# Kernel optimization log

Hardware: AMD Instinct MI355X
Metric: run time of the kernel (lower is better)

The kernel has to match this reference:

```python
import jax, jax.numpy as jnp
import numpy as np

H, HKV, D, HID = 32, 8, 128, 4096
L, CTX, S = 64, 64, 8192
T = CTX + L
HALF = D // 2
EPS = 1e-6
WP = 4096


def setup_inputs() -> dict:
    key = jax.random.key(0)
    ks = jax.random.split(key, 16)
    f = jnp.float32
    w = 0.02
    return {
        "x": jax.random.normal(ks[0], (1, L, HID), f),
        "x_ctx": jax.random.normal(ks[1], (1, CTX, HID), f),
        "cos_q": jax.random.uniform(ks[2], (1, 1, L, HALF), f, -1.0, 1.0),
        "sin_q": jax.random.uniform(ks[3], (1, 1, L, HALF), f, -1.0, 1.0),
        "cos_k": jax.random.uniform(ks[4], (1, 1, T, HALF), f, -1.0, 1.0),
        "sin_k": jax.random.uniform(ks[5], (1, 1, T, HALF), f, -1.0, 1.0),
        "cache_K_in": jax.random.normal(ks[6], (1, HKV, S, D), f),
        "cache_V_in": jax.random.normal(ks[7], (1, HKV, S, D), f),
        "causal_mask": jnp.ones((1, 1, L, WP + T), dtype=bool),
        "Wq": jax.random.normal(ks[8], (HID, H * D), f) * w,
        "Wk": jax.random.normal(ks[9], (HID, HKV * D), f) * w,
        "Wv": jax.random.normal(ks[10], (HID, HKV * D), f) * w,
        "Wo": jax.random.normal(ks[11], (H * D, HID), f) * w,
        "q_norm_w": jnp.ones((D,), f),
        "k_norm_w": jnp.ones((D,), f),
        "write_pos": WP,
        "rotate": 0,
    }


def _rmsnorm(x, w):
    # normalize over head_dim (last axis)
    var = jnp.mean(x * x, axis=-1, keepdims=True)
    return x * jax.lax.rsqrt(var + EPS) * w


def _rope(x, cos, sin):
    # x: (B, H, T, D); cos/sin: (1, 1, T, HALF) -- rotate-half convention
    x1, x2 = x[..., :HALF], x[..., HALF:]
    return jnp.concatenate([x1 * cos - x2 * sin, x2 * cos + x1 * sin], axis=-1)


def reference(x, x_ctx, cos_q, sin_q, cos_k, sin_k, cache_K_in, cache_V_in,
              causal_mask, Wq, Wk, Wv, Wo, q_norm_w, k_norm_w, write_pos, rotate):
    c = jnp.concatenate([x_ctx, x], axis=1)                  # (1, T, HID)
    q = (x @ Wq).reshape(1, L, H, D)
    k = (c @ Wk).reshape(1, T, HKV, D)
    v = (c @ Wv).reshape(1, T, HKV, D)
    q = _rmsnorm(q, q_norm_w).transpose(0, 2, 1, 3)          # (1, H, L, D)
    k = _rmsnorm(k, k_norm_w).transpose(0, 2, 1, 3)          # (1, HKV, T, D)
    v = v.transpose(0, 2, 1, 3)                               # (1, HKV, T, D)
    q = _rope(q, cos_q, sin_q)
    k = _rope(k, cos_k, sin_k)

    if rotate:  # static Python branch (rotate is a compile-time constant)
        attend_K = jnp.concatenate([cache_K_in[:, :, T:S], k], axis=2)
        attend_V = jnp.concatenate([cache_V_in[:, :, T:S], v], axis=2)
    elif write_pos == 0:
        attend_K, attend_V = k, v
    else:
        attend_K = jnp.concatenate([cache_K_in[:, :, :write_pos], k], axis=2)
        attend_V = jnp.concatenate([cache_V_in[:, :, :write_pos], v], axis=2)

    rep = H // HKV
    scale = jnp.float32(D) ** -0.5
    qg = q.reshape(1, HKV, rep, L, D)
    # grouped attention: broadcast KV heads inline instead of materializing expand
    scores = jnp.einsum('bgrld,bgad->bgrla', qg, attend_K) * scale
    scores = jnp.where(causal_mask[:, :, None], scores, -jnp.inf)  # (1,1,1,L,A) bcast
    probs = jax.nn.softmax(scores, axis=-1)
    o = jnp.einsum('bgrla,bgad->bgrld', probs, attend_V)     # (1, HKV, rep, L, D)
    o = o.reshape(1, H, L, D).transpose(0, 2, 1, 3).reshape(1, L, H * D)
    return (o @ Wo, k, v)
```

## Files before the change

kernel.cpp:

```cpp
#include <hip/hip_runtime.h>

typedef unsigned short u16;
typedef __bf16 bf16x8 __attribute__((ext_vector_type(8)));
typedef float f32x4 __attribute__((ext_vector_type(4)));
typedef u16 u16x8 __attribute__((ext_vector_type(8)));

#define NSPLIT 22
#define KSPLIT 4
#define KC 1024
#define NKT 16
#define OSPLIT 8
#define SCALE_Q 0.08838834764831843f

__device__ __forceinline__ u16 f2bf(float f) {
    unsigned u = __builtin_bit_cast(unsigned, f);
    u += 0x7fff + ((u >> 16) & 1);
    return (u16)(u >> 16);
}
__device__ __forceinline__ float bf2f(u16 h) {
    unsigned u = ((unsigned)h) << 16;
    return __builtin_bit_cast(float, u);
}
__device__ __forceinline__ f32x4 mfma16(bf16x8 a, bf16x8 b, f32x4 c) {
    return __builtin_amdgcn_mfma_f32_16x16x32_bf16(a, b, c, 0, 0, 0);
}

__global__ __launch_bounds__(256)
void k_qkv(const float* __restrict__ x, const float* __restrict__ xctx,
           const float* __restrict__ Wq, const float* __restrict__ Wk,
           const float* __restrict__ Wv, float* __restrict__ part)
{
    const int col0 = blockIdx.x * 32;
    const int ksp = blockIdx.y;
    const int ks0 = ksp * KC;
    const float* W; int ldw, cbase, mat;
    if (col0 < 4096)      { W = Wq; ldw = 4096; cbase = col0;        mat = 0; }
    else if (col0 < 5120) { W = Wk; ldw = 1024; cbase = col0 - 4096; mat = 1; }
    else                  { W = Wv; ldw = 1024; cbase = col0 - 5120; mat = 2; }
    const bool full = (mat != 0);
    const int rowbase = full ? 0 : 64;

    __shared__ __align__(16) u16 As[128][72];
    __shared__ __align__(16) u16 Bs[32 * 64];

    const int t = threadIdx.x;
    const int w = t >> 6, l = t & 63;
    const int lm = l & 15, lg = l >> 4;

    const int arow_base = t >> 4;
    const int akk = (t & 15) << 2;
    const int bk = (t >> 3) << 1;
    const int bn4 = (t & 7) << 2;

    f32x4 pa[8]; f32x4 pb[2];
    f32x4 acc[2][2] = {};

    const float* xr = x - (size_t)64 * 4096;

    #define QKV_LOAD(kt_)                                                      \
    {                                                                          \
        const int kg = ks0 + (kt_) * 64;                                       \
        _Pragma("unroll")                                                      \
        for (int it = 0; it < 4; it++) {                                       \
            int grow = rowbase + it * 16 + arow_base;                          \
            const float* src = (grow < 64) ? (xctx + (size_t)grow * 4096)      \
                                           : (xr + (size_t)grow * 4096);       \
            pa[it] = *(const f32x4*)&src[kg + akk];                            \
        }                                                                      \
        if (full) {                                                            \
            _Pragma("unroll")                                                  \
            for (int it = 4; it < 8; it++) {                                   \
                int grow = it * 16 + arow_base;                                \
                const float* src = (grow < 64) ? (xctx + (size_t)grow * 4096)  \
                                               : (xr + (size_t)grow * 4096);   \
                pa[it] = *(const f32x4*)&src[kg + akk];                        \
            }                                                                  \
        }                                                                      \
        _Pragma("unroll")                                                      \
        for (int e = 0; e < 2; e++)                                            \
            pb[e] = *(const f32x4*)&W[(size_t)(kg + bk + e) * ldw + cbase + bn4]; \
    }

    #define QKV_STORE()                                                        \
    {                                                                          \
        _Pragma("unroll")                                                      \
        for (int it = 0; it < 4; it++) {                                       \
            ushort4 sv; sv.x = f2bf(pa[it][0]); sv.y = f2bf(pa[it][1]);        \
            sv.z = f2bf(pa[it][2]); sv.w = f2bf(pa[it][3]);                    \
            *(ushort4*)&As[it * 16 + arow_base][akk] = sv;                     \
        }                                                                      \
        if (full) {                                                            \
            _Pragma("unroll")                                                  \
            for (int it = 4; it < 8; it++) {                                   \
                ushort4 sv; sv.x = f2bf(pa[it][0]); sv.y = f2bf(pa[it][1]);    \
                sv.z = f2bf(pa[it][2]); sv.w = f2bf(pa[it][3]);                \
                *(ushort4*)&As[it * 16 + arow_base][akk] = sv;                 \
            }                                                                  \
        }                                                                      \
        _Pragma("unroll")                                                      \
        for (int j = 0; j < 4; j++) {                                          \
            int n = bn4 + j;                                                   \
            int idx = n * 64 + (bk ^ (((n >> 1) & 7) << 3));                   \
            ushort2 v2; v2.x = f2bf(pb[0][j]); v2.y = f2bf(pb[1][j]);          \
            *(ushort2*)&Bs[idx] = v2;                                          \
        }                                                                      \
    }

    QKV_LOAD(0);
    #pragma unroll 1
    for (int kt = 0; kt < NKT; kt++) {
        if (kt) __syncthreads();
        QKV_STORE();
        __syncthreads();
        if (kt + 1 < NKT) QKV_LOAD(kt + 1);
        #pragma unroll
        for (int ks = 0; ks < 2; ks++) {
            const int koff = ks * 32 + lg * 8;
            bf16x8 bfr[2];
            #pragma unroll
            for (int nt = 0; nt < 2; nt++) {
                int n = nt * 16 + lm;
                bfr[nt] = *(const bf16x8*)&Bs[n * 64 + (koff ^ (((n >> 1) & 7) << 3))];
            }
            bf16x8 a0 = *(const bf16x8*)&As[w * (full ? 32 : 16) + lm][koff];
            acc[0][0] = mfma16(a0, bfr[0], acc[0][0]);
            acc[0][1] = mfma16(a0, bfr[1], acc[0][1]);
            if (full) {
                bf16x8 a1 = *(const bf16x8*)&As[w * 32 + 16 + lm][koff];
                acc[1][0] = mfma16(a1, bfr[0], acc[1][0]);
                acc[1][1] = mfma16(a1, bfr[1], acc[1][1]);
            }
        }
    }

    const int wrows = full ? 32 : 16;
    const int mts = full ? 2 : 1;
    #pragma unroll
    for (int mt = 0; mt < 2; mt++) {
        if (mt >= mts) break;
        #pragma unroll
        for (int nt = 0; nt < 2; nt++)
            #pragma unroll
            for (int r = 0; r < 4; r++) {
                int grow = rowbase + w * wrows + mt * 16 + lg * 4 + r;
                part[((size_t)ksp * 128 + grow) * 6144 + col0 + nt * 16 + lm] =
                    acc[mt][nt][r];
            }
    }
    #undef QKV_LOAD
    #undef QKV_STORE
}

__global__ __launch_bounds__(256)
void k_normrope(const float* __restrict__ part,
                const float* __restrict__ cosq, const float* __restrict__ sinq,
                const float* __restrict__ cosk, const float* __restrict__ sink,
                const float* __restrict__ qnw, const float* __restrict__ knw,
                u16* __restrict__ qb, u16* __restrict__ kb,
                float* __restrict__ outk, float* __restrict__ outv,
                u16* __restrict__ vbw)
{
    int wid = blockIdx.x * 4 + (threadIdx.x >> 6);
    int lane = threadIdx.x & 63;
    if (wid < 2048) {
        int h = wid >> 6, lq = wid & 63;
        size_t ro = (size_t)(64 + lq) * 6144 + h * 128;
        float x1 = 0.f, x2 = 0.f;
        #pragma unroll
        for (int s = 0; s < KSPLIT; s++) {
            x1 += part[(size_t)s * 786432 + ro + lane];
            x2 += part[(size_t)s * 786432 + ro + lane + 64];
        }
        float ss = x1 * x1 + x2 * x2;
        #pragma unroll
        for (int off = 32; off; off >>= 1) ss += __shfl_xor(ss, off);
        float rms = rsqrtf(ss * (1.0f / 128.0f) + 1e-6f);
        float a = x1 * rms * qnw[lane];
        float b = x2 * rms * qnw[lane + 64];
        float c = cosq[lq * 64 + lane], s = sinq[lq * 64 + lane];
        u16* qo = qb + ((size_t)h * 64 + lq) * 128;
        qo[lane]      = f2bf((a * c - b * s) * SCALE_Q);
        qo[lane + 64] = f2bf((b * c + a * s) * SCALE_Q);
    } else if (wid < 3072) {
        int rr = wid - 2048;
        int kh = rr >> 7, tt = rr & 127;
        size_t ro = (size_t)tt * 6144 + 4096 + kh * 128;
        float x1 = 0.f, x2 = 0.f;
        #pragma unroll
        for (int s = 0; s < KSPLIT; s++) {
            x1 += part[(size_t)s * 786432 + ro + lane];
            x2 += part[(size_t)s * 786432 + ro + lane + 64];
        }
        float ss = x1 * x1 + x2 * x2;
        #pragma unroll
        for (int off = 32; off; off >>= 1) ss += __shfl_xor(ss, off);
        float rms = rsqrtf(ss * (1.0f / 128.0f) + 1e-6f);
        float a = x1 * rms * knw[lane];
        float b = x2 * rms * knw[lane + 64];
        float c = cosk[tt * 64 + lane], s = sink[tt * 64 + lane];
        float o1 = a * c - b * s, o2 = b * c + a * s;
        size_t oi = ((size_t)kh * 128 + tt) * 128;
        outk[oi + lane] = o1; outk[oi + lane + 64] = o2;
        kb[oi + lane] = f2bf(o1); kb[oi + lane + 64] = f2bf(o2);
    } else {
        int rr = wid - 3072;
        int kh = rr >> 7, tt = rr & 127;
        size_t ro = (size_t)tt * 6144 + 5120 + kh * 128;
        float v1 = 0.f, v2 = 0.f;
        #pragma unroll
        for (int s = 0; s < KSPLIT; s++) {
            v1 += part[(size_t)s * 786432 + ro + lane];
            v2 += part[(size_t)s * 786432 + ro + lane + 64];
        }
        size_t oi = ((size_t)kh * 128 + tt) * 128;
        outv[oi + lane] = v1; outv[oi + lane + 64] = v2;
        vbw[oi + lane] = f2bf(v1); vbw[oi + lane + 64] = f2bf(v2);
    }
}

__global__ __launch_bounds__(256)
void k_attn(const u16* __restrict__ qb, const u16* __restrict__ kbw,
            const u16* __restrict__ vbw,
            const float* __restrict__ cacheK, const float* __restrict__ cacheV,
            u16* __restrict__ opart, float* __restrict__ lpart)
{
    const int split = blockIdx.x;
    const int kh = blockIdx.y;
    const int t = threadIdx.x;
    const int w = t >> 6, l = t & 63;
    const int lm = l & 15, lg = l >> 4;

    __shared__ __align__(16) u16 Ks[64][136];
    __shared__ __align__(16) u16 Vs[128][72];
    __shared__ __align__(16) u16 Ps[4][64][40];

    const u16* qh = qb + ((size_t)(kh * 4 + w) * 64) * 128;
    bf16x8 aq[4][4];
    #pragma unroll
    for (int mt = 0; mt < 4; mt++)
        #pragma unroll
        for (int ks = 0; ks < 4; ks++)
            aq[mt][ks] = *(const bf16x8*)&qh[(size_t)(mt * 16 + lm) * 128 + ks * 32 + lg * 8];

    f32x4 accO[4][8] = {};
    float lacc[4][4] = {};
    const size_t khK = (size_t)kh * 8192 * 128;

    for (int kbi = 0; kbi < 3; kbi++) {
        const int key0 = split * 192 + kbi * 64;
        __syncthreads();
        #pragma unroll
        for (int it = 0; it < 8; it++) {
            int fidx = it * 256 + t;
            int row = fidx >> 5;
            int d4 = (fidx & 31) << 2;
            int key = key0 + row;
            if (key < 4096) {
                float4 kv = *(const float4*)&cacheK[khK + (size_t)key * 128 + d4];
                ushort4 sv; sv.x = f2bf(kv.x); sv.y = f2bf(kv.y);
                sv.z = f2bf(kv.z); sv.w = f2bf(kv.w);
                *(ushort4*)&Ks[row][d4] = sv;
                float4 vv = *(const float4*)&cacheV[khK + (size_t)key * 128 + d4];
                Vs[d4 + 0][row] = f2bf(vv.x);
                Vs[d4 + 1][row] = f2bf(vv.y);
                Vs[d4 + 2][row] = f2bf(vv.z);
                Vs[d4 + 3][row] = f2bf(vv.w);
            } else {
                size_t nb = ((size_t)kh * 128 + (key - 4096)) * 128 + d4;
                ushort4 kv = *(const ushort4*)&kbw[nb];
                *(ushort4*)&Ks[row][d4] = kv;
                ushort4 vv = *(const ushort4*)&vbw[nb];
                Vs[d4 + 0][row] = vv.x;
                Vs[d4 + 1][row] = vv.y;
                Vs[d4 + 2][row] = vv.z;
                Vs[d4 + 3][row] = vv.w;
            }
        }
        __syncthreads();

        f32x4 sa[4][4] = {};
        #pragma unroll
        for (int ks = 0; ks < 4; ks++) {
            bf16x8 bk[4];
            #pragma unroll
            for (int nt = 0; nt < 4; nt++)
                bk[nt] = *(const bf16x8*)&Ks[nt * 16 + lm][ks * 32 + lg * 8];
            #pragma unroll
            for (int mt = 0; mt < 4; mt++)
                #pragma unroll
                for (int nt = 0; nt < 4; nt++)
                    sa[mt][nt] = mfma16(aq[mt][ks], bk[nt], sa[mt][nt]);
        }

        #pragma unroll
        for (int half = 0; half < 2; half++) {
            __syncthreads();
            #pragma unroll
            for (int mt = 0; mt < 4; mt++)
                #pragma unroll
                for (int nt2 = 0; nt2 < 2; nt2++)
                    #pragma unroll
                    for (int r = 0; r < 4; r++) {
                        float e = __expf(sa[mt][half * 2 + nt2][r]);
                        lacc[mt][r] += e;
                        Ps[w][mt * 16 + lg * 4 + r][nt2 * 16 + lm] = f2bf(e);
                    }
            __syncthreads();
            bf16x8 pa[4];
            #pragma unroll
            for (int mt = 0; mt < 4; mt++)
                pa[mt] = *(const bf16x8*)&Ps[w][mt * 16 + lm][lg * 8];
            #pragma unroll
            for (int dt = 0; dt < 8; dt++) {
                bf16x8 vb8 = *(const bf16x8*)&Vs[dt * 16 + lm][half * 32 + lg * 8];
                #pragma unroll
                for (int mt = 0; mt < 4; mt++)
                    accO[mt][dt] = mfma16(pa[mt], vb8, accO[mt][dt]);
            }
        }
    }

    #pragma unroll
    for (int mt = 0; mt < 4; mt++)
        #pragma unroll
        for (int r = 0; r < 4; r++) {
            float v = lacc[mt][r];
            v += __shfl_xor(v, 1);
            v += __shfl_xor(v, 2);
            v += __shfl_xor(v, 4);
            v += __shfl_xor(v, 8);
            lacc[mt][r] = v;
        }

    const size_t base = (((size_t)kh * NSPLIT + split) * 4 + w) * 64;
    if (lm == 0) {
        #pragma unroll
        for (int mt = 0; mt < 4; mt++)
            #pragma unroll
            for (int r = 0; r < 4; r++)
                lpart[base + mt * 16 + lg * 4 + r] = lacc[mt][r];
    }
    #pragma unroll
    for (int mt = 0; mt < 4; mt++)
        #pragma unroll
        for (int dt = 0; dt < 8; dt++)
            #pragma unroll
            for (int r = 0; r < 4; r++)
                opart[(base + mt * 16 + lg * 4 + r) * 128 + dt * 16 + lm] =
                    f2bf(accO[mt][dt][r]);
}

__global__ __launch_bounds__(256)
void k_combine(const u16* __restrict__ opart, const float* __restrict__ lpart,
               u16* __restrict__ obf)
{
    int idx = blockIdx.x * 256 + threadIdx.x;
    int lq = idx >> 12;
    int col = idx & 4095;
    int h = col >> 7, d = col & 127;
    int kh = h >> 2, rep = h & 3;
    float os = 0.f, ls = 0.f;
    for (int s = 0; s < NSPLIT; s++) {
        size_t b = (((size_t)kh * NSPLIT + s) * 4 + rep) * 64 + lq;
        os += bf2f(opart[b * 128 + d]);
        ls += lpart[b];
    }
    obf[idx] = f2bf(os / ls);
}

__global__ __launch_bounds__(256)
void k_oproj(const u16* __restrict__ obf, const float* __restrict__ Wo,
             float* __restrict__ parto)
{
    const int col0 = blockIdx.x * 32;
    const int osp = blockIdx.y;
    const int ks0 = osp * (4096 / OSPLIT);

    __shared__ __align__(16) u16 As[64][72];
    __shared__ __align__(16) u16 Bs[32 * 64];

    const int t = threadIdx.x;
    const int w = t >> 6, l = t & 63;
    const int lm = l & 15, lg = l >> 4;

    const int arow = t >> 3;
    const int ac8 = (t & 7) << 3;
    const int bk = (t >> 3) << 1;
    const int bn4 = (t & 7) << 2;

    u16x8 pa[2]; f32x4 pb[2];
    f32x4 acc[2] = {};

    #define OP_LOAD(kt_)                                                       \
    {                                                                          \
        const int kg = ks0 + (kt_) * 64;                                       \
        pa[0] = *(const u16x8*)&obf[(size_t)arow * 4096 + kg + ac8];           \
        pa[1] = *(const u16x8*)&obf[(size_t)(arow + 32) * 4096 + kg + ac8];    \
        pb[0] = *(const f32x4*)&Wo[(size_t)(kg + bk) * 4096 + col0 + bn4];     \
        pb[1] = *(const f32x4*)&Wo[(size_t)(kg + bk + 1) * 4096 + col0 + bn4]; \
    }

    #define OP_STORE()                                                         \
    {                                                                          \
        *(u16x8*)&As[arow][ac8] = pa[0];                                       \
        *(u16x8*)&As[arow + 32][ac8] = pa[1];                                  \
        _Pragma("unroll")                                                      \
        for (int j = 0; j < 4; j++) {                                          \
            int n = bn4 + j;                                                   \
            int idx = n * 64 + (bk ^ (((n >> 1) & 7) << 3));                   \
            ushort2 v2; v2.x = f2bf(pb[0][j]); v2.y = f2bf(pb[1][j]);          \
            *(ushort2*)&Bs[idx] = v2;                                          \
        }                                                                      \
    }

    OP_LOAD(0);
    #pragma unroll 1
    for (int kt = 0; kt < 4096 / OSPLIT / 64; kt++) {
        if (kt) __syncthreads();
        OP_STORE();
        __syncthreads();
        if (kt + 1 < 4096 / OSPLIT / 64) OP_LOAD(kt + 1);
        #pragma unroll
        for (int ks = 0; ks < 2; ks++) {
            const int koff = ks * 32 + lg * 8;
            bf16x8 a0 = *(const bf16x8*)&As[w * 16 + lm][koff];
            #pragma unroll
            for (int nt = 0; nt < 2; nt++) {
                int n = nt * 16 + lm;
                bf16x8 b = *(const bf16x8*)&Bs[n * 64 + (koff ^ (((n >> 1) & 7) << 3))];
                acc[nt] = mfma16(a0, b, acc[nt]);
            }
        }
    }
    #pragma unroll
    for (int nt = 0; nt < 2; nt++)
        #pragma unroll
        for (int r = 0; r < 4; r++)
            parto[((size_t)osp * 64 + w * 16 + lg * 4 + r) * 4096 +
                  col0 + nt * 16 + lm] = acc[nt][r];
    #undef OP_LOAD
    #undef OP_STORE
}

__global__ __launch_bounds__(256)
void k_osum(const float* __restrict__ parto, float* __restrict__ out0)
{
    int idx = blockIdx.x * 256 + threadIdx.x;
    float s = 0.f;
    #pragma unroll
    for (int o = 0; o < OSPLIT; o++)
        s += parto[(size_t)o * 262144 + idx];
    out0[idx] = s;
}

extern "C" void kernel_launch(void* const* d_in, const int* in_sizes, int n_in,
                              void* d_out, int out_size, void* d_ws, size_t ws_size,
                              hipStream_t stream)
{
    (void)in_sizes; (void)n_in; (void)out_size; (void)ws_size;
    const float* x      = (const float*)d_in[0];
    const float* xctx   = (const float*)d_in[1];
    const float* cosq   = (const float*)d_in[2];
    const float* sinq   = (const float*)d_in[3];
    const float* cosk   = (const float*)d_in[4];
    const float* sink   = (const float*)d_in[5];
    const float* cacheK = (const float*)d_in[6];
    const float* cacheV = (const float*)d_in[7];
    const float* Wq     = (const float*)d_in[9];
    const float* Wk     = (const float*)d_in[10];
    const float* Wv     = (const float*)d_in[11];
    const float* Wo     = (const float*)d_in[12];
    const float* qnw    = (const float*)d_in[13];
    const float* knw    = (const float*)d_in[14];

    float* out0 = (float*)d_out;
    float* out1 = out0 + 262144;
    float* out2 = out1 + 131072;

    char* ws = (char*)d_ws;
    float* part  = (float*)(ws + 0);
    u16*   opart = (u16*)(ws + 0);
    float* lpart = (float*)(ws + 11534336);
    float* parto = (float*)(ws + 0);
    u16*   qb    = (u16*)(ws + 12582912);
    u16*   kb    = (u16*)(ws + 13107200);
    u16*   vb    = (u16*)(ws + 13369344);
    u16*   obf   = (u16*)(ws + 13631488);

    k_qkv<<<dim3(192, KSPLIT), 256, 0, stream>>>(x, xctx, Wq, Wk, Wv, part);
    k_normrope<<<1024, 256, 0, stream>>>(part, cosq, sinq, cosk, sink,
                                         qnw, knw, qb, kb, out1, out2, vb);
    k_attn<<<dim3(NSPLIT, 8), 256, 0, stream>>>(qb, kb, vb, cacheK, cacheV, opart, lpart);
    k_combine<<<1024, 256, 0, stream>>>(opart, lpart, obf);
    k_oproj<<<dim3(128, OSPLIT), 256, 0, stream>>>(obf, Wo, parto);
    k_osum<<<1024, 256, 0, stream>>>(parto, out0);
}
```

Baseline: 86.73 us.

## Pre-convert activations to bf16 MFMA fragment layout in a separate prep kernel

Adds a k_prep kernel that converts x and x_ctx once to bf16 and stores them in a layout matching the MFMA A-fragment order. The QKV GEMM then reads its A operands straight from global memory, with no shared-memory staging and no per-block fp32-to-bf16 conversion. This removes the redundant activation loads and conversions repeated across all 192 column blocks, and halves LDS use. The cost is an extra kernel launch and uncoalesced-style fragment reads that rely on L2 hits. It also adds an unroll pragma to the combine loop.

```diff
diff --git a/kernel.cpp b/kernel.cpp
--- a/kernel.cpp
+++ b/kernel.cpp
@@ -26,7 +26,29 @@
 }
 
 __global__ __launch_bounds__(256)
-void k_qkv(const float* __restrict__ x, const float* __restrict__ xctx,
+void k_prep(const float* __restrict__ x, const float* __restrict__ xctx,
+            u16* __restrict__ fragA)
+{
+    int tid = blockIdx.x * 256 + threadIdx.x;
+    int row = tid >> 9;
+    int kc = tid & 511;
+    int k0 = kc << 3;
+    const float* src = (row < 64) ? (xctx + (size_t)row * 4096)
+                                  : (x + (size_t)(row - 64) * 4096);
+    f32x4 v0 = *(const f32x4*)&src[k0];
+    f32x4 v1 = *(const f32x4*)&src[k0 + 4];
+    u16x8 o;
+    o[0] = f2bf(v0[0]); o[1] = f2bf(v0[1]); o[2] = f2bf(v0[2]); o[3] = f2bf(v0[3]);
+    o[4] = f2bf(v1[0]); o[5] = f2bf(v1[1]); o[6] = f2bf(v1[2]); o[7] = f2bf(v1[3]);
+    int ks32 = k0 >> 5;
+    int lg = (k0 >> 3) & 3;
+    int rt = row >> 4;
+    int l = lg * 16 + (row & 15);
+    *(u16x8*)&fragA[(((size_t)ks32 * 8 + rt) * 64 + l) * 8] = o;
+}
+
+__global__ __launch_bounds__(256)
+void k_qkv(const u16* __restrict__ fragA,
            const float* __restrict__ Wq, const float* __restrict__ Wk,
            const float* __restrict__ Wv, float* __restrict__ part)
 {
@@ -40,63 +62,29 @@
     const bool full = (mat != 0);
     const int rowbase = full ? 0 : 64;
 
-    __shared__ __align__(16) u16 As[128][72];
     __shared__ __align__(16) u16 Bs[32 * 64];
 
     const int t = threadIdx.x;
     const int w = t >> 6, l = t & 63;
     const int lm = l & 15, lg = l >> 4;
 
-    const int arow_base = t >> 4;
-    const int akk = (t & 15) << 2;
     const int bk = (t >> 3) << 1;
     const int bn4 = (t & 7) << 2;
 
-    f32x4 pa[8]; f32x4 pb[2];
+    f32x4 pb[2];
     f32x4 acc[2][2] = {};
 
-    const float* xr = x - (size_t)64 * 4096;
-
-    #define QKV_LOAD(kt_)                                                      \
+    const int rt0 = full ? (w * 2) : (4 + w);
+
+    #define QKV_BLOAD(kt_)                                                     \
     {                                                                          \
         const int kg = ks0 + (kt_) * 64;                                       \
-        _Pragma("unroll")                                                      \
-        for (int it = 0; it < 4; it++) {                                       \
-            int grow = rowbase + it * 16 + arow_base;                          \
-            const float* src = (grow < 64) ? (xctx + (size_t)grow * 4096)      \
-                                           : (xr + (size_t)grow * 4096);       \
-            pa[it] = *(const f32x4*)&src[kg + akk];                            \
-        }                                                                      \
-        if (full) {                                                            \
-            _Pragma("unroll")                                                  \
-            for (int it = 4; it < 8; it++) {                                   \
-                int grow = it * 16 + arow_base;                                \
-                const float* src = (grow < 64) ? (xctx + (size_t)grow * 4096)  \
-                                               : (xr + (size_t)grow * 4096);   \
-                pa[it] = *(const f32x4*)&src[kg + akk];                        \
-            }                                                                  \
-        }                                                                      \
-        _Pragma("unroll")                                                      \
-        for (int e = 0; e < 2; e++)                                            \
-            pb[e] = *(const f32x4*)&W[(size_t)(kg + bk + e) * ldw + cbase + bn4]; \
-    }
-
-    #define QKV_STORE()                                                        \
+        pb[0] = *(const f32x4*)&W[(size_t)(kg + bk) * ldw + cbase + bn4];      \
+        pb[1] = *(const f32x4*)&W[(size_t)(kg + bk + 1) * ldw + cbase + bn4];  \
+    }
+
+    #define QKV_BSTORE()                                                       \
     {                                                                          \
-        _Pragma("unroll")                                                      \
-        for (int it = 0; it < 4; it++) {                                       \
-            ushort4 sv; sv.x = f2bf(pa[it][0]); sv.y = f2bf(pa[it][1]);        \
-            sv.z = f2bf(pa[it][2]); sv.w = f2bf(pa[it][3]);                    \
-            *(ushort4*)&As[it * 16 + arow_base][akk] = sv;                     \
-        }                                                                      \
-        if (full) {                                                            \
-            _Pragma("unroll")                                                  \
-            for (int it = 4; it < 8; it++) {                                   \
-                ushort4 sv; sv.x = f2bf(pa[it][0]); sv.y = f2bf(pa[it][1]);    \
-                sv.z = f2bf(pa[it][2]); sv.w = f2bf(pa[it][3]);                \
-                *(ushort4*)&As[it * 16 + arow_base][akk] = sv;                 \
-            }                                                                  \
-        }                                                                      \
         _Pragma("unroll")                                                      \
         for (int j = 0; j < 4; j++) {                                          \
             int n = bn4 + j;                                                   \
@@ -106,27 +94,30 @@
         }                                                                      \
     }
 
-    QKV_LOAD(0);
+    QKV_BLOAD(0);
     #pragma unroll 1
     for (int kt = 0; kt < NKT; kt++) {
         if (kt) __syncthreads();
-        QKV_STORE();
+        QKV_BSTORE();
         __syncthreads();
-        if (kt + 1 < NKT) QKV_LOAD(kt + 1);
+        if (kt + 1 < NKT) QKV_BLOAD(kt + 1);
+        const int ks32b = (ks0 >> 5) + kt * 2;
         #pragma unroll
         for (int ks = 0; ks < 2; ks++) {
             const int koff = ks * 32 + lg * 8;
+            bf16x8 a0 = *(const bf16x8*)
+                &fragA[(((size_t)(ks32b + ks) * 8 + rt0) * 64 + l) * 8];
             bf16x8 bfr[2];
             #pragma unroll
             for (int nt = 0; nt < 2; nt++) {
                 int n = nt * 16 + lm;
                 bfr[nt] = *(const bf16x8*)&Bs[n * 64 + (koff ^ (((n >> 1) & 7) << 3))];
             }
-            bf16x8 a0 = *(const bf16x8*)&As[w * (full ? 32 : 16) + lm][koff];
             acc[0][0] = mfma16(a0, bfr[0], acc[0][0]);
             acc[0][1] = mfma16(a0, bfr[1], acc[0][1]);
             if (full) {
-                bf16x8 a1 = *(const bf16x8*)&As[w * 32 + 16 + lm][koff];
+                bf16x8 a1 = *(const bf16x8*)
+                    &fragA[(((size_t)(ks32b + ks) * 8 + rt0 + 1) * 64 + l) * 8];
                 acc[1][0] = mfma16(a1, bfr[0], acc[1][0]);
                 acc[1][1] = mfma16(a1, bfr[1], acc[1][1]);
             }
@@ -147,8 +138,8 @@
                     acc[mt][nt][r];
             }
     }
-    #undef QKV_LOAD
-    #undef QKV_STORE
+    #undef QKV_BLOAD
+    #undef QKV_BSTORE
 }
 
 __global__ __launch_bounds__(256)
@@ -360,6 +351,7 @@
     int h = col >> 7, d = col & 127;
     int kh = h >> 2, rep = h & 3;
     float os = 0.f, ls = 0.f;
+    #pragma unroll 2
     for (int s = 0; s < NSPLIT; s++) {
         size_t b = (((size_t)kh * NSPLIT + s) * 4 + rep) * 64 + lq;
         os += bf2f(opart[b * 128 + d]);
@@ -482,15 +474,18 @@
     u16*   opart = (u16*)(ws + 0);
     float* lpart = (float*)(ws + 11534336);
     float* parto = (float*)(ws + 0);
+    u16*   fragA = (u16*)(ws + 12582912);
     u16*   qb    = (u16*)(ws + 12582912);
     u16*   kb    = (u16*)(ws + 13107200);
     u16*   vb    = (u16*)(ws + 13369344);
     u16*   obf   = (u16*)(ws + 13631488);
 
-    k_qkv<<<dim3(192, KSPLIT), 256, 0, stream>>>(x, xctx, Wq, Wk, Wv, part);
+    k_prep<<<256, 256, 0, stream>>>(x, xctx, fragA);
+    k_qkv<<<dim3(192, KSPLIT), 256, 0, stream>>>(fragA, Wq, Wk, Wv, part);
     k_normrope<<<1024, 256, 0, stream>>>(part, cosq, sinq, cosk, sink,
                                          qnw, knw, qb, kb, out1, out2, vb);
-    k_attn<<<dim3(NSPLIT, 8), 256, 0, stream>>>(qb, kb, vb, cacheK, cacheV, opart, lpart);
+    k_attn<<<dim3(NSPLIT, 8), 256, 0, stream>>>(qb, kb, vb, cacheK, cacheV,
+                                                opart, lpart);
     k_combine<<<1024, 256, 0, stream>>>(opart, lpart, obf);
     k_oproj<<<dim3(128, OSPLIT), 256, 0, stream>>>(obf, Wo, parto);
     k_osum<<<1024, 256, 0, stream>>>(parto, out0);
```

Result: slower. 94.48 us (+8.9%).
